# Optimization experiments

Hardware: AMD Instinct MI355X
Metric: run time of the kernel (lower is better)

Reference implementation:

```python
import jax, jax.numpy as jnp
import numpy as np

EMBED_DIM = 1024
NUM_HEADS = 16
HEAD_DIM = EMBED_DIM // NUM_HEADS


def setup_inputs() -> dict:
    key = jax.random.key(0)
    k1, k2, k3, k4 = jax.random.split(key, 4)
    x = jax.random.normal(k1, (2, 2048, EMBED_DIM), dtype=jnp.float32)
    # nn.Linear weights: stored as [out, in]; we keep that convention.
    s = 1.0 / np.sqrt(EMBED_DIM)
    w_qkv = jax.random.uniform(k2, (3 * EMBED_DIM, EMBED_DIM), jnp.float32, -s, s)
    w_proj = jax.random.uniform(k3, (EMBED_DIM, EMBED_DIM), jnp.float32, -s, s)
    b_proj = jax.random.uniform(k4, (EMBED_DIM,), jnp.float32, -s, s)
    return {"x": x, "w_qkv": w_qkv, "w_proj": w_proj, "b_proj": b_proj}


def reference(x, w_qkv, w_proj, b_proj):
    B, N, C = x.shape
    H, D = NUM_HEADS, HEAD_DIM
    scale = D ** -0.5
    # qkv: [B, N, 3C] -> [3, B, H, N, D]
    qkv = jnp.einsum('bnc,oc->bno', x, w_qkv)
    qkv = qkv.reshape(B, N, 3, H, D).transpose(2, 0, 3, 1, 4)
    q, k, v = qkv[0] * scale, qkv[1], qkv[2]
    attn = jax.nn.softmax(jnp.einsum('bhnd,bhmd->bhnm', q, k), axis=-1)
    out = jnp.einsum('bhnm,bhmd->bhnd', attn, v)
    out = out.transpose(0, 2, 1, 3).reshape(B, N, C)
    return jnp.einsum('bnc,oc->bno', out, w_proj) + b_proj
```

## Files before the change

### kernel.cpp

```cpp
#include <hip/hip_runtime.h>


constexpr int B_ = 2, N_ = 2048, C_ = 1024, H_ = 16, D_ = 64;
constexpr int M_ = B_ * N_;
constexpr int O3 = 3 * C_;
constexpr int KVB = 64;
constexpr int NTILES = N_ / KVB;

typedef short bf16x8 __attribute__((ext_vector_type(8)));
typedef _Float16 half8 __attribute__((ext_vector_type(8)));
typedef _Float16 half4v __attribute__((ext_vector_type(4)));
typedef float f32x4  __attribute__((ext_vector_type(4)));
typedef float f32x16 __attribute__((ext_vector_type(16)));

__device__ __forceinline__ unsigned short f2bf(float f) {
    unsigned int u = __float_as_uint(f);
    unsigned int r = (u + 0x7FFFu + ((u >> 16) & 1u)) >> 16;
    return (unsigned short)r;
}

__device__ __forceinline__ float fexp2(float x) {
    float r;
    asm("v_exp_f32 %0, %1" : "=v"(r) : "v"(x));
    return r;
}

__device__ __forceinline__ void async16(const void* g, void* l) {
    __builtin_amdgcn_global_load_lds(
        (const __attribute__((address_space(1))) unsigned int*)g,
        (__attribute__((address_space(3))) unsigned int*)l, 16, 0, 0);
}

constexpr size_t XN  = (size_t)M_ * C_;
constexpr size_t WQN = (size_t)O3 * C_;
constexpr size_t WPN = (size_t)C_ * C_;

__global__ __launch_bounds__(256)
void convert_f16(const float* __restrict__ x, const float* __restrict__ wq,
                 const float* __restrict__ wp, _Float16* __restrict__ dst)
{
    size_t i = ((size_t)blockIdx.x * 256 + threadIdx.x) * 8;
    const float* src;
    size_t off;
    if (i < XN)            { src = x;  off = i; }
    else if (i < XN + WQN) { src = wq; off = i - XN; }
    else                   { src = wp; off = i - XN - WQN; }
    float4 a = *(const float4*)(src + off);
    float4 b = *(const float4*)(src + off + 4);
    half8 h;
    h[0] = (_Float16)a.x; h[1] = (_Float16)a.y; h[2] = (_Float16)a.z; h[3] = (_Float16)a.w;
    h[4] = (_Float16)b.x; h[5] = (_Float16)b.y; h[6] = (_Float16)b.z; h[7] = (_Float16)b.w;
    *(half8*)(dst + i) = h;
}

template<int MODE>
__global__ __launch_bounds__(256)
void gemm128(const _Float16* __restrict__ Ag, const _Float16* __restrict__ Bg,
             unsigned short* __restrict__ Qd, unsigned short* __restrict__ Kd,
             unsigned short* __restrict__ Vt,
             const float* __restrict__ bias, float* __restrict__ Out)
{
    __shared__ __align__(16) unsigned char Ab[2][16384];
    __shared__ __align__(16) unsigned char Bb[2][16384];

    const int t    = threadIdx.x;
    const int lane = t & 63;
    const int w    = t >> 6;
    const int g    = lane >> 4;
    const int c    = lane & 15;
    const int wm   = w >> 1, wn = w & 1;
    const int bm   = blockIdx.y * 128;
    const int bn   = blockIdx.x * 128;
    constexpr int K = C_;

    f32x4 acc[4][4];
    f32x4 zero = {0.f, 0.f, 0.f, 0.f};
    #pragma unroll
    for (int mi = 0; mi < 4; ++mi)
        #pragma unroll
        for (int ni = 0; ni < 4; ++ni) acc[mi][ni] = zero;

    auto stage = [&](int buf, int k0) {
        #pragma unroll
        for (int i = 0; i < 4; ++i) {
            int id  = t + 256 * i;
            int row = id >> 3;
            int p   = id & 7;
            int gs  = p ^ (row & 7);
            async16(Ag + (size_t)(bm + row) * K + k0 + 8 * gs, &Ab[buf][id * 16]);
            async16(Bg + (size_t)(bn + row) * K + k0 + 8 * gs, &Bb[buf][id * 16]);
        }
    };

    stage(0, 0);
    __syncthreads();
    int cur = 0;

    for (int k0 = 0; k0 < K; k0 += 64) {
        if (k0 + 64 < K) stage(cur ^ 1, k0 + 64);

        const unsigned char* Abase = Ab[cur];
        const unsigned char* Bbase = Bb[cur];
        #pragma unroll
        for (int s = 0; s < 2; ++s) {
            half8 af[4], bf[4];
            #pragma unroll
            for (int mi = 0; mi < 4; ++mi) {
                int row = wm * 64 + mi * 16 + c;
                af[mi] = *(const half8*)(Abase + (row * 8 + ((s * 4 + g) ^ (row & 7))) * 16);
            }
            #pragma unroll
            for (int ni = 0; ni < 4; ++ni) {
                int row = wn * 64 + ni * 16 + c;
                bf[ni] = *(const half8*)(Bbase + (row * 8 + ((s * 4 + g) ^ (row & 7))) * 16);
            }
            #pragma unroll
            for (int mi = 0; mi < 4; ++mi)
                #pragma unroll
                for (int ni = 0; ni < 4; ++ni)
                    acc[mi][ni] = __builtin_amdgcn_mfma_f32_16x16x32_f16(af[mi], bf[ni], acc[mi][ni], 0, 0, 0);
        }

        __syncthreads();
        cur ^= 1;
    }

    if constexpr (MODE == 0) {
        constexpr float QSCALE = 0.125f * 1.4426950408889634f;
        const int o0 = bn + wn * 64;
        const int which = o0 >> 10;
        const int h  = (o0 & 1023) >> 6;
        const int m0 = bm + wm * 64;
        const int b  = m0 >> 11;
        const int n0 = m0 & 2047;
        const size_t bh = (size_t)b * H_ + h;
        if (which == 0) {
            unsigned short* base = Qd + (bh * N_) * D_;
            #pragma unroll
            for (int mi = 0; mi < 4; ++mi)
                #pragma unroll
                for (int ni = 0; ni < 4; ++ni)
                    #pragma unroll
                    for (int r = 0; r < 4; ++r)
                        base[(size_t)(n0 + mi * 16 + 4 * g + r) * D_ + ni * 16 + c] =
                            f2bf(acc[mi][ni][r] * QSCALE);
        } else if (which == 1) {
            unsigned short* base = Kd + (bh * N_) * D_;
            #pragma unroll
            for (int mi = 0; mi < 4; ++mi)
                #pragma unroll
                for (int ni = 0; ni < 4; ++ni)
                    #pragma unroll
                    for (int r = 0; r < 4; ++r)
                        base[(size_t)(n0 + mi * 16 + 4 * g + r) * D_ + ni * 16 + c] =
                            f2bf(acc[mi][ni][r]);
        } else {
            unsigned short* base = Vt + (bh * D_) * (size_t)N_;
            #pragma unroll
            for (int mi = 0; mi < 4; ++mi)
                #pragma unroll
                for (int ni = 0; ni < 4; ++ni) {
                    ushort4 v;
                    v.x = f2bf(acc[mi][ni][0]);
                    v.y = f2bf(acc[mi][ni][1]);
                    v.z = f2bf(acc[mi][ni][2]);
                    v.w = f2bf(acc[mi][ni][3]);
                    *(ushort4*)&base[(size_t)(ni * 16 + c) * N_ + n0 + mi * 16 + 4 * g] = v;
                }
        }
    } else {
        const int m0 = bm + wm * 64;
        const int o0 = bn + wn * 64;
        #pragma unroll
        for (int ni = 0; ni < 4; ++ni) {
            float bb = bias[o0 + ni * 16 + c];
            #pragma unroll
            for (int mi = 0; mi < 4; ++mi)
                #pragma unroll
                for (int r = 0; r < 4; ++r)
                    Out[(size_t)(m0 + mi * 16 + 4 * g + r) * C_ + o0 + ni * 16 + c] =
                        acc[mi][ni][r] + bb;
        }
    }
}

__global__ __launch_bounds__(256, 2)
void attn_mfma(const unsigned short* __restrict__ Qd, const unsigned short* __restrict__ Kd,
               const unsigned short* __restrict__ Vt, _Float16* __restrict__ AO)
{
    __shared__ __align__(16) unsigned char KsB[2][8192];
    __shared__ __align__(16) unsigned char VtB[2][8192];

    const int t    = threadIdx.x;
    const int lane = t & 63;
    const int w    = t >> 6;
    const int h    = lane >> 5;
    const int q31  = lane & 31;
    const int qsw  = q31 & 7;

    int flat = blockIdx.x;
    int work = (flat & 7) * 64 + (flat >> 3);
    const int bh = work >> 4;
    const int qt = work & 15;
    const int b  = bh >> 4, hh = bh & 15;
    const int q0 = qt * 128;

    const unsigned short* Kp = Kd + (size_t)bh * N_ * D_;
    const unsigned short* Vp = Vt + (size_t)bh * D_ * N_;

    const unsigned short* qp = Qd + ((size_t)bh * N_ + q0 + w * 32 + q31) * D_;
    bf16x8 qf[4];
    #pragma unroll
    for (int s = 0; s < 4; ++s)
        qf[s] = *(const bf16x8*)(qp + 16 * s + 8 * h);

    int go[4];
    #pragma unroll
    for (int s = 0; s < 4; ++s) go[s] = ((2 * s + h) ^ qsw) << 4;
    const int row0off = q31 * 128;
    const int row1off = (32 + q31) * 128;

    const int rk = t >> 3, pk = t & 7;
    const unsigned char* kSrc = (const unsigned char*)Kp + rk * 128 + ((pk ^ (rk & 7)) << 4);
    const unsigned char* vSrc = (const unsigned char*)Vp + (size_t)rk * (N_ * 2) + ((pk ^ (rk & 7)) << 4);
    unsigned char* kDstA = KsB[0] + t * 16;
    unsigned char* kDstB = KsB[1] + t * 16;
    unsigned char* vDstA = VtB[0] + t * 16;
    unsigned char* vDstB = VtB[1] + t * 16;

    float m_run = -1e30f, l_run = 0.f;
    f32x16 oc0 = 0.f, oc1 = 0.f;

    auto stage = [&](unsigned char* kD, unsigned char* vD, int kt) {
        async16(kSrc + (size_t)kt * 8192, kD);
        async16(kSrc + (size_t)kt * 8192 + 4096, kD + 4096);
        async16(vSrc + (size_t)kt * 128, vD);
        async16(vSrc + 32 * (size_t)(N_ * 2) + (size_t)kt * 128, vD + 4096);
    };

    stage(kDstA, vDstA, 0);
    __syncthreads();

    auto tile_body = [&](const unsigned char* kbase, const unsigned char* vbase,
                         unsigned char* kDstN, unsigned char* vDstN, int ktNext) {
        if (ktNext < NTILES) stage(kDstN, vDstN, ktNext);

        f32x16 st0 = 0.f, st1 = 0.f;
        const unsigned char* krow0 = kbase + row0off;
        const unsigned char* krow1 = kbase + row1off;
        __builtin_amdgcn_s_setprio(1);
        #pragma unroll
        for (int s = 0; s < 4; ++s) {
            bf16x8 a0 = *(const bf16x8*)(krow0 + go[s]);
            bf16x8 a1 = *(const bf16x8*)(krow1 + go[s]);
            st0 = __builtin_amdgcn_mfma_f32_32x32x16_bf16(a0, qf[s], st0, 0, 0, 0);
            st1 = __builtin_amdgcn_mfma_f32_32x32x16_bf16(a1, qf[s], st1, 0, 0, 0);
        }
        __builtin_amdgcn_s_setprio(0);

        f32x16 mm;
        #pragma unroll
        for (int r = 0; r < 16; ++r) mm[r] = fmaxf(st0[r], st1[r]);
        float a0 = fmaxf(fmaxf(mm[0], mm[1]), mm[2]);
        float a1 = fmaxf(fmaxf(mm[3], mm[4]), mm[5]);
        float a2 = fmaxf(fmaxf(mm[6], mm[7]), mm[8]);
        float a3 = fmaxf(fmaxf(mm[9], mm[10]), mm[11]);
        float a4 = fmaxf(fmaxf(mm[12], mm[13]), mm[14]);
        float mx = fmaxf(fmaxf(fmaxf(a0, a1), fmaxf(a2, a3)), fmaxf(a4, mm[15]));
        mx = fmaxf(mx, __shfl_xor(mx, 32));

        const bool defer = __all(mx <= m_run + 8.f);
        if (!defer) {
            const float nm = fmaxf(m_run, mx);
            const float corr = fexp2(m_run - nm);
            m_run = nm;
            oc0 *= corr;
            oc1 *= corr;
            l_run *= corr;
        }
        #pragma unroll
        for (int r = 0; r < 16; ++r) {
            st0[r] = fexp2(st0[r] - m_run);
            st1[r] = fexp2(st1[r] - m_run);
        }

        f32x16 sv = st0 + st1;
        float ts = ((sv[0] + sv[1]) + (sv[2] + sv[3])) + ((sv[4] + sv[5]) + (sv[6] + sv[7]))
                 + ((sv[8] + sv[9]) + (sv[10] + sv[11])) + ((sv[12] + sv[13]) + (sv[14] + sv[15]));
        ts += __shfl_xor(ts, 32);
        l_run += ts;

        unsigned int pkd[2][4][2];
        #pragma unroll
        for (int m = 0; m < 4; ++m)
            #pragma unroll
            for (int j = 0; j < 2; ++j) {
                pkd[0][m][j] = __byte_perm(__float_as_uint(st0[4*m + 2*j]),
                                           __float_as_uint(st0[4*m + 2*j + 1]), 0x7632);
                pkd[1][m][j] = __byte_perm(__float_as_uint(st1[4*m + 2*j]),
                                           __float_as_uint(st1[4*m + 2*j + 1]), 0x7632);
            }

        #pragma unroll
        for (int kb = 0; kb < 2; ++kb)
            #pragma unroll
            for (int u = 0; u < 2; ++u)
                #pragma unroll
                for (int j = 0; j < 2; ++j)
                    asm("v_permlane32_swap_b32 %0, %1"
                        : "+v"(pkd[kb][2*u][j]), "+v"(pkd[kb][2*u+1][j]));

        bf16x8 pb[4];
        #pragma unroll
        for (int s = 0; s < 4; ++s) {
            const int kb = s >> 1, u = s & 1;
            union { unsigned int d[4]; bf16x8 v; } uu;
            uu.d[0] = pkd[kb][2*u][0];
            uu.d[1] = pkd[kb][2*u][1];
            uu.d[2] = pkd[kb][2*u+1][0];
            uu.d[3] = pkd[kb][2*u+1][1];
            pb[s] = uu.v;
        }

        const unsigned char* vrow0 = vbase + row0off;
        const unsigned char* vrow1 = vbase + row1off;
        __builtin_amdgcn_s_setprio(1);
        #pragma unroll
        for (int s = 0; s < 4; ++s) {
            bf16x8 va0 = *(const bf16x8*)(vrow0 + go[s]);
            bf16x8 va1 = *(const bf16x8*)(vrow1 + go[s]);
            oc0 = __builtin_amdgcn_mfma_f32_32x32x16_bf16(va0, pb[s], oc0, 0, 0, 0);
            oc1 = __builtin_amdgcn_mfma_f32_32x32x16_bf16(va1, pb[s], oc1, 0, 0, 0);
        }
        __builtin_amdgcn_s_setprio(0);

        __syncthreads();
    };

    #pragma unroll 1
    for (int kt = 0; kt < NTILES; kt += 2) {
        tile_body(KsB[0], VtB[0], kDstB, vDstB, kt + 1);
        tile_body(KsB[1], VtB[1], kDstA, vDstA, kt + 2);
    }

    float inv = 1.0f / l_run;
    const int q = q0 + w * 32 + q31;
    _Float16* aop = AO + ((size_t)b * N_ + q) * C_ + hh * D_;
    #pragma unroll
    for (int m = 0; m < 4; ++m) {
        half4v o0, o1;
        #pragma unroll
        for (int i = 0; i < 4; ++i) {
            o0[i] = (_Float16)(oc0[4*m + i] * inv);
            o1[i] = (_Float16)(oc1[4*m + i] * inv);
        }
        *(half4v*)(aop + 8 * m + 4 * h) = o0;
        *(half4v*)(aop + 32 + 8 * m + 4 * h) = o1;
    }
}

extern "C" void kernel_launch(void* const* d_in, const int* in_sizes, int n_in,
                              void* d_out, int out_size, void* d_ws, size_t ws_size,
                              hipStream_t stream) {
    const float* x      = (const float*)d_in[0];
    const float* w_qkv  = (const float*)d_in[1];
    const float* w_proj = (const float*)d_in[2];
    const float* b_proj = (const float*)d_in[3];
    float* out = (float*)d_out;

    const size_t hd = (size_t)B_ * H_ * N_ * D_;
    unsigned short* Qd = (unsigned short*)d_ws;
    unsigned short* Kd = Qd + hd;
    unsigned short* Vt = Kd + hd;
    _Float16* AO  = (_Float16*)(Vt + hd);
    _Float16* x16 = AO + hd;
    _Float16* wq16 = x16 + XN;
    _Float16* wp16 = wq16 + WQN;

    convert_f16<<<4096, 256, 0, stream>>>(x, w_qkv, w_proj, x16);
    gemm128<0><<<dim3(O3 / 128, M_ / 128), 256, 0, stream>>>(
        x16, wq16, Qd, Kd, Vt, nullptr, nullptr);
    attn_mfma<<<dim3(512), 256, 0, stream>>>(Qd, Kd, Vt, AO);
    gemm128<1><<<dim3(C_ / 128, M_ / 128), 256, 0, stream>>>(
        AO, wp16, nullptr, nullptr, nullptr, b_proj, out);
}
```

Before: 124.0 us.

## Split attention KV range across two wave groups and merge partial softmax

The attention block doubles to 512 threads. Two groups of four waves each process half of the KV tiles for the same 128 queries, each with its own double-buffered K/V shared memory. At the end, group 1 writes its partial output accumulators, running max and sum to shared memory, and group 0 rescales and combines them before writing fp16 output. This raises the number of waves per CU to hide latency in the KV loop, at the cost of doubled LDS use, higher register pressure under launch_bounds(512,4), and an extra merge step.

```diff
diff --git a/kernel.cpp b/kernel.cpp
--- a/kernel.cpp
+++ b/kernel.cpp
@@ -184,16 +184,19 @@
     }
 }
 
-__global__ __launch_bounds__(256, 2)
+__global__ __launch_bounds__(512, 4)
 void attn_mfma(const unsigned short* __restrict__ Qd, const unsigned short* __restrict__ Kd,
                const unsigned short* __restrict__ Vt, _Float16* __restrict__ AO)
 {
-    __shared__ __align__(16) unsigned char KsB[2][8192];
-    __shared__ __align__(16) unsigned char VtB[2][8192];
+    __shared__ __align__(16) unsigned char Kbuf[2][2][8192];
+    __shared__ __align__(16) unsigned char Vbuf[2][2][8192];
 
     const int t    = threadIdx.x;
     const int lane = t & 63;
     const int w    = t >> 6;
+    const int wg   = w >> 2;
+    const int wl   = w & 3;
+    const int tl   = t & 255;
     const int h    = lane >> 5;
     const int q31  = lane & 31;
     const int qsw  = q31 & 7;
@@ -208,7 +211,7 @@
     const unsigned short* Kp = Kd + (size_t)bh * N_ * D_;
     const unsigned short* Vp = Vt + (size_t)bh * D_ * N_;
 
-    const unsigned short* qp = Qd + ((size_t)bh * N_ + q0 + w * 32 + q31) * D_;
+    const unsigned short* qp = Qd + ((size_t)bh * N_ + q0 + wl * 32 + q31) * D_;
     bf16x8 qf[4];
     #pragma unroll
     for (int s = 0; s < 4; ++s)
@@ -220,13 +223,17 @@
     const int row0off = q31 * 128;
     const int row1off = (32 + q31) * 128;
 
-    const int rk = t >> 3, pk = t & 7;
+    const int rk = tl >> 3, pk = tl & 7;
     const unsigned char* kSrc = (const unsigned char*)Kp + rk * 128 + ((pk ^ (rk & 7)) << 4);
     const unsigned char* vSrc = (const unsigned char*)Vp + (size_t)rk * (N_ * 2) + ((pk ^ (rk & 7)) << 4);
-    unsigned char* kDstA = KsB[0] + t * 16;
-    unsigned char* kDstB = KsB[1] + t * 16;
-    unsigned char* vDstA = VtB[0] + t * 16;
-    unsigned char* vDstB = VtB[1] + t * 16;
+    unsigned char* kDstA = Kbuf[wg][0] + tl * 16;
+    unsigned char* kDstB = Kbuf[wg][1] + tl * 16;
+    unsigned char* vDstA = Vbuf[wg][0] + tl * 16;
+    unsigned char* vDstB = Vbuf[wg][1] + tl * 16;
+    const unsigned char* kb0 = Kbuf[wg][0];
+    const unsigned char* kb1 = Kbuf[wg][1];
+    const unsigned char* vb0 = Vbuf[wg][0];
+    const unsigned char* vb1 = Vbuf[wg][1];
 
     float m_run = -1e30f, l_run = 0.f;
     f32x16 oc0 = 0.f, oc1 = 0.f;
@@ -238,12 +245,13 @@
         async16(vSrc + 32 * (size_t)(N_ * 2) + (size_t)kt * 128, vD + 4096);
     };
 
-    stage(kDstA, vDstA, 0);
+    const int kt0 = wg * 16, ktEnd = kt0 + 16;
+    stage(kDstA, vDstA, kt0);
     __syncthreads();
 
     auto tile_body = [&](const unsigned char* kbase, const unsigned char* vbase,
                          unsigned char* kDstN, unsigned char* vDstN, int ktNext) {
-        if (ktNext < NTILES) stage(kDstN, vDstN, ktNext);
+        if (ktNext < ktEnd) stage(kDstN, vDstN, ktNext);
 
         f32x16 st0 = 0.f, st1 = 0.f;
         const unsigned char* krow0 = kbase + row0off;
@@ -338,24 +346,46 @@
     };
 
     #pragma unroll 1
-    for (int kt = 0; kt < NTILES; kt += 2) {
-        tile_body(KsB[0], VtB[0], kDstB, vDstB, kt + 1);
-        tile_body(KsB[1], VtB[1], kDstA, vDstA, kt + 2);
+    for (int kt = kt0; kt < ktEnd; kt += 2) {
+        tile_body(kb0, vb0, kDstB, vDstB, kt + 1);
+        tile_body(kb1, vb1, kDstA, vDstA, kt + 2);
     }
 
-    float inv = 1.0f / l_run;
-    const int q = q0 + w * 32 + q31;
-    _Float16* aop = AO + ((size_t)b * N_ + q) * C_ + hh * D_;
-    #pragma unroll
-    for (int m = 0; m < 4; ++m) {
-        half4v o0, o1;
-        #pragma unroll
-        for (int i = 0; i < 4; ++i) {
-            o0[i] = (_Float16)(oc0[4*m + i] * inv);
-            o1[i] = (_Float16)(oc1[4*m + i] * inv);
-        }
-        *(half4v*)(aop + 8 * m + 4 * h) = o0;
-        *(half4v*)(aop + 32 + 8 * m + 4 * h) = o1;
+    float* cb = (float*)&Kbuf[0][0][0];
+    if (wg == 1) {
+        float* s = cb + tl * 40;
+        #pragma unroll
+        for (int m = 0; m < 4; ++m) {
+            f32x4 a, bq;
+            #pragma unroll
+            for (int i = 0; i < 4; ++i) { a[i] = oc0[4*m + i]; bq[i] = oc1[4*m + i]; }
+            *(f32x4*)(s + 4 * m) = a;
+            *(f32x4*)(s + 16 + 4 * m) = bq;
+        }
+        s[32] = m_run;
+        s[33] = l_run;
+    }
+    __syncthreads();
+    if (wg == 0) {
+        const float* s = cb + tl * 40;
+        float m1 = s[32], l1 = s[33];
+        float mm = fmaxf(m_run, m1);
+        float c0 = fexp2(m_run - mm);
+        float c1 = fexp2(m1 - mm);
+        float inv = 1.0f / (l_run * c0 + l1 * c1);
+        const int q = q0 + wl * 32 + q31;
+        _Float16* aop = AO + ((size_t)b * N_ + q) * C_ + hh * D_;
+        #pragma unroll
+        for (int m = 0; m < 4; ++m) {
+            half4v o0, o1;
+            #pragma unroll
+            for (int i = 0; i < 4; ++i) {
+                o0[i] = (_Float16)((oc0[4*m + i] * c0 + s[4*m + i] * c1) * inv);
+                o1[i] = (_Float16)((oc1[4*m + i] * c0 + s[16 + 4*m + i] * c1) * inv);
+            }
+            *(half4v*)(aop + 8 * m + 4 * h) = o0;
+            *(half4v*)(aop + 32 + 8 * m + 4 * h) = o1;
+        }
     }
 }
 
@@ -380,7 +410,7 @@
     convert_f16<<<4096, 256, 0, stream>>>(x, w_qkv, w_proj, x16);
     gemm128<0><<<dim3(O3 / 128, M_ / 128), 256, 0, stream>>>(
         x16, wq16, Qd, Kd, Vt, nullptr, nullptr);
-    attn_mfma<<<dim3(512), 256, 0, stream>>>(Qd, Kd, Vt, AO);
+    attn_mfma<<<dim3(512), 512, 0, stream>>>(Qd, Kd, Vt, AO);
     gemm128<1><<<dim3(C_ / 128, M_ / 128), 256, 0, stream>>>(
         AO, wp16, nullptr, nullptr, nullptr, b_proj, out);
 }
```

Measured after the change: 121.0 us. 2.4% less time.
